# Kernel tuning notes

Hardware: AMD Instinct MI355X
Metric: run time of the kernel (lower is better)

Reference implementation:

```python
import jax, jax.numpy as jnp
import numpy as np

B, S, D, H = 4, 2048, 1024, 16
HD = D // H  # head_dim = 64


def setup_inputs() -> dict:
    key = jax.random.key(0)
    ks = jax.random.split(key, 5)
    scale = 0.02
    x = jax.random.normal(ks[0], (B, S, D), dtype=jnp.float32)
    W_qkv = jax.random.normal(ks[1], (D, 3 * D), dtype=jnp.float32) * scale
    b_qkv = jnp.zeros((3 * D,), dtype=jnp.float32)
    W_out = jax.random.normal(ks[2], (D, D), dtype=jnp.float32) * scale
    b_out = jnp.zeros((D,), dtype=jnp.float32)
    return {"x": x, "W_qkv": W_qkv, "b_qkv": b_qkv, "W_out": W_out, "b_out": b_out}


def reference(x, W_qkv, b_qkv, W_out, b_out):
    b, s, d = x.shape
    qkv = x @ W_qkv + b_qkv                      # [B,S,3D]
    q, k, v = jnp.split(qkv, 3, axis=-1)
    # [B,S,D] -> [B,H,S,hd]
    q = q.reshape(b, s, H, HD).transpose(0, 2, 1, 3)
    k = k.reshape(b, s, H, HD).transpose(0, 2, 1, 3)
    v = v.reshape(b, s, H, HD).transpose(0, 2, 1, 3)
    scores = jnp.einsum('bhqd,bhkd->bhqk', q, k) / jnp.sqrt(jnp.float32(HD))
    causal = jnp.tril(jnp.ones((s, s), dtype=bool))  # [S,S]
    scores = jnp.where(causal[None, None], scores, -jnp.inf)
    probs = jax.nn.softmax(scores, axis=-1)
    # dropout is identity in eval mode
    attn = jnp.einsum('bhqk,bhkd->bhqd', probs, v)  # [B,H,S,hd]
    attn = attn.transpose(0, 2, 1, 3).reshape(b, s, d)
    return attn @ W_out + b_out
```

## Files before the change

kernel.cpp:

```cpp
#include <hip/hip_runtime.h>


typedef short s16;
typedef __attribute__((ext_vector_type(4))) short s16x4;
typedef __attribute__((ext_vector_type(8))) short bf16x8;
typedef __attribute__((ext_vector_type(4))) float f32x4;

__device__ __forceinline__ s16 f2bf(float f) {
    union { float f; unsigned int i; } v;
    v.f = f;
    unsigned int r = v.i + 0x7fffu + ((v.i >> 16) & 1u);
    return (s16)(r >> 16);
}

__device__ __forceinline__ unsigned pack_bf16(float a, float b) {
    union { float f; unsigned u; } x, y;
    x.f = a; y.f = b;
    return __byte_perm(x.u + 0x8000u, y.u + 0x8000u, 0x7632);
}

__device__ __forceinline__ void load_lds16(const s16* g, s16* lds_base) {
    __builtin_amdgcn_global_load_lds(
        (const __attribute__((address_space(1))) void*)g,
        (__attribute__((address_space(3))) void*)lds_base, 16, 0, 0);
}

__global__ void cast_f32_bf16(const float* __restrict__ in, s16* __restrict__ out) {
    const int i = (blockIdx.x * 256 + threadIdx.x) * 4;
    const float4 f = *(const float4*)(in + i);
    s16x4 r = {f2bf(f.x), f2bf(f.y), f2bf(f.z), f2bf(f.w)};
    *(s16x4*)(out + i) = r;
}

__global__ void transpose_cast(const float* __restrict__ in,
                               s16* __restrict__ out, int R, int C) {
    __shared__ float tile[32][33];
    const int cb = blockIdx.x * 32, rb = blockIdx.y * 32;
    const int tx = threadIdx.x, ty = threadIdx.y;
#pragma unroll
    for (int i = 0; i < 32; i += 8)
        tile[ty + i][tx] = in[(size_t)(rb + ty + i) * C + cb + tx];
    __syncthreads();
#pragma unroll
    for (int i = 0; i < 32; i += 8)
        out[(size_t)(cb + ty + i) * R + rb + tx] = f2bf(tile[tx][ty + i]);
}

template <bool OUT_F32>
__global__ __launch_bounds__(512, 2) void gemm_bt_bias_256(
    const s16* __restrict__ A,
    const s16* __restrict__ Bt,
    const float* __restrict__ bias,
    void* __restrict__ Cv,
    int M, int N, int K, int gx) {
    __shared__ __attribute__((aligned(16))) s16 As[2][256 * 64];
    __shared__ __attribute__((aligned(16))) s16 Bs[2][256 * 64];

    const int tid  = threadIdx.x;
    const int lane = tid & 63;
    const int wave = tid >> 6;
    const int l15  = lane & 15;
    const int quad = lane >> 4;
    const int wr   = wave >> 2;
    const int wc   = wave & 3;

    const int cpx = (int)gridDim.x >> 3;
    const int bid = (int)blockIdx.x;
    const int swz = (bid & 7) * cpx + (bid >> 3);
    const int m0 = (swz / gx) * 256;
    const int n0 = (swz % gx) * 256;

    const int srow = tid >> 3;
    const int sg   = (tid & 7) ^ (srow & 7);
    const s16* Ag = A  + (size_t)(m0 + srow) * K + sg * 8;
    const s16* Bg = Bt + (size_t)(n0 + srow) * K + sg * 8;

#define STG(buf, c, kt) do {                                                        \
    load_lds16(Ag + (size_t)(c) * 64 * K + (size_t)(kt) * 64,                       \
               &As[buf][(c) * 4096 + wave * 512]);                                  \
    load_lds16(Bg + (size_t)(c) * 64 * K + (size_t)(kt) * 64,                       \
               &Bs[buf][(c) * 4096 + wave * 512]); } while (0)

    f32x4 acc[8][4];
#pragma unroll
    for (int i = 0; i < 8; ++i)
#pragma unroll
        for (int j = 0; j < 4; ++j)
            acc[i][j] = (f32x4){0.f, 0.f, 0.f, 0.f};

    const int nk = K >> 6;

    STG(0, 0, 0); STG(0, 1, 0); STG(0, 2, 0); STG(0, 3, 0);
    __syncthreads();

    for (int t = 0; t < nk; ++t) {
        const int buf  = t & 1;
        const int nbuf = buf ^ 1;
        const bool pre = (t + 1 < nk);
        bf16x8 bfr[4][2];
#pragma unroll
        for (int q = 0; q < 4; ++q) {
            if (q == 0) {
#pragma unroll
                for (int n = 0; n < 4; ++n)
#pragma unroll
                    for (int ks = 0; ks < 2; ++ks) {
                        const int br = wc * 64 + n * 16 + l15;
                        const int gs = ((ks * 4 + quad) ^ (l15 & 7)) * 8;
                        bfr[n][ks] = *(const bf16x8*)(&Bs[buf][br * 64 + gs]);
                    }
            }
            bf16x8 af[2][2];
#pragma unroll
            for (int i = 0; i < 2; ++i)
#pragma unroll
                for (int ks = 0; ks < 2; ++ks) {
                    const int ar = wr * 128 + (q * 2 + i) * 16 + l15;
                    const int gs = ((ks * 4 + quad) ^ (l15 & 7)) * 8;
                    af[i][ks] = *(const bf16x8*)(&As[buf][ar * 64 + gs]);
                }
            if (q == 0 && pre) { STG(nbuf, 0, t + 1); STG(nbuf, 1, t + 1); }
            if (q == 1 && pre) { STG(nbuf, 2, t + 1); STG(nbuf, 3, t + 1); }
            __builtin_amdgcn_s_barrier();
            __builtin_amdgcn_s_setprio(1);
#pragma unroll
            for (int i = 0; i < 2; ++i)
#pragma unroll
                for (int n = 0; n < 4; ++n)
#pragma unroll
                    for (int ks = 0; ks < 2; ++ks)
                        acc[q * 2 + i][n] = __builtin_amdgcn_mfma_f32_16x16x32_bf16(
                            af[i][ks], bfr[n][ks], acc[q * 2 + i][n], 0, 0, 0);
            __builtin_amdgcn_s_setprio(0);
            if (q == 3)
                __syncthreads();
            else
                __builtin_amdgcn_s_barrier();
        }
    }
#undef STG

#pragma unroll
    for (int n = 0; n < 4; ++n) {
        const int col = n0 + wc * 64 + n * 16 + l15;
        const float bv = bias[col];
#pragma unroll
        for (int mf = 0; mf < 8; ++mf) {
            const int rowb = m0 + wr * 128 + mf * 16 + quad * 4;
#pragma unroll
            for (int r = 0; r < 4; ++r) {
                const float v = acc[mf][n][r] + bv;
                if constexpr (OUT_F32)
                    ((float*)Cv)[(size_t)(rowb + r) * N + col] = v;
                else
                    ((s16*)Cv)[(size_t)(rowb + r) * N + col] = f2bf(v);
            }
        }
    }
}

__global__ __launch_bounds__(256) void attn_fwd(
    const s16* __restrict__ qkv,
    s16* __restrict__ attn) {
    __shared__ __attribute__((aligned(16))) s16 Ks[64 * 72];
    __shared__ __attribute__((aligned(16))) s16 Vt[64 * 72];
    __shared__ __attribute__((aligned(16))) s16 PT[4][32][88];

    const int tid  = threadIdx.x;
    const int lane = tid & 63;
    const int wave = tid >> 6;
    const int l15  = lane & 15;
    const int quad = lane >> 4;

    const int bid = blockIdx.x;
    const int hi  = bid >> 8;
    const int a   = bid & 3;
    const int bh  = (bid >> 2) & 63;
    const int qbase = a * 2 + (hi >> 1);
    const int qt  = (hi & 1) ? 15 - qbase : qbase;

    const size_t rowbase = (size_t)(bh >> 4) * 2048;
    const int hoff = (bh & 15) * 64;
    const int kp  = tid >> 3;
    const int p_s = tid & 7;
    const int kg  = kp >> 2;

    const float C2 = 0.18033688011112042f;
    const float M2 = 12.0f;

    const int wq = qt * 128 + wave * 32;

    bf16x8 qf[2][2];
#pragma unroll
    for (int qs = 0; qs < 2; ++qs)
#pragma unroll
        for (int ks = 0; ks < 2; ++ks)
            qf[qs][ks] = *(const bf16x8*)(qkv + (rowbase + wq + qs * 16 + l15) * 3072 + hoff + ks * 32 + quad * 8);

    float l_lane[2] = {0.f, 0.f};
    f32x4 o[2][4];
#pragma unroll
    for (int qs = 0; qs < 2; ++qs)
#pragma unroll
        for (int hs = 0; hs < 4; ++hs)
            o[qs][hs] = (f32x4){0.f, 0.f, 0.f, 0.f};

    const int nkt = qt * 2 + 2;
    bf16x8 kv[2], vv[2];
#pragma unroll
    for (int dk = 0; dk < 2; ++dk) {
        const s16* g = qkv + (rowbase + 2 * kp + dk) * 3072 + hoff + p_s * 8;
        kv[dk] = *(const bf16x8*)(g + 1024);
        vv[dk] = *(const bf16x8*)(g + 2048);
    }

    for (int kt = 0; kt < nkt; ++kt) {
        const int k0 = kt * 64;
        __syncthreads();
#pragma unroll
        for (int dk = 0; dk < 2; ++dk)
            *(bf16x8*)(Ks + (2 * kp + dk) * 72 + p_s * 8) = kv[dk];
#pragma unroll
        for (int j = 0; j < 8; ++j) {
            const unsigned dw = (unsigned)(unsigned short)vv[0][j] |
                                ((unsigned)(unsigned short)vv[1][j] << 16);
            *(unsigned*)(Vt + (p_s * 8 + j) * 72 + ((kg ^ p_s) << 3) + (2 * kp & 7)) = dw;
        }
        __syncthreads();

        if (kt + 1 < nkt) {
#pragma unroll
            for (int dk = 0; dk < 2; ++dk) {
                const s16* g = qkv + (rowbase + k0 + 64 + 2 * kp + dk) * 3072 + hoff + p_s * 8;
                kv[dk] = *(const bf16x8*)(g + 1024);
                vv[dk] = *(const bf16x8*)(g + 2048);
            }
        }

        if (k0 > wq + 31) continue;

        f32x4 st[2][4];
#pragma unroll
        for (int qs = 0; qs < 2; ++qs)
#pragma unroll
            for (int kb = 0; kb < 4; ++kb)
                st[qs][kb] = (f32x4){0.f, 0.f, 0.f, 0.f};
        __builtin_amdgcn_s_setprio(1);
#pragma unroll
        for (int kb = 0; kb < 4; ++kb)
#pragma unroll
            for (int ks = 0; ks < 2; ++ks) {
                const bf16x8 kf = *(const bf16x8*)(Ks + (kb * 16 + l15) * 72 + ks * 32 + quad * 8);
#pragma unroll
                for (int qs = 0; qs < 2; ++qs)
                    st[qs][kb] = __builtin_amdgcn_mfma_f32_16x16x32_bf16(kf, qf[qs][ks], st[qs][kb], 0, 0, 0);
            }
        __builtin_amdgcn_s_setprio(0);

        const bool edge = (k0 + 63 > wq);
#pragma unroll
        for (int qs = 0; qs < 2; ++qs) {
            const int q = wq + qs * 16 + l15;
#pragma unroll
            for (int kb = 0; kb < 4; ++kb) {
                float p4[4];
#pragma unroll
                for (int r = 0; r < 4; ++r) {
                    float t = fmaf(st[qs][kb][r], C2, -M2);
                    if (edge) {
                        const int key = k0 + kb * 16 + quad * 4 + r;
                        t = (key <= q) ? t : -150.f;
                    }
                    p4[r] = __builtin_amdgcn_exp2f(t);
                    l_lane[qs] += p4[r];
                }
                uint2 dd;
                dd.x = pack_bf16(p4[0], p4[1]);
                dd.y = pack_bf16(p4[2], p4[3]);
                *(uint2*)(&PT[wave][qs * 16 + l15][kb * 16 + quad * 4]) = dd;
            }
        }

        __builtin_amdgcn_s_setprio(1);
#pragma unroll
        for (int kk = 0; kk < 2; ++kk) {
            bf16x8 pf[2];
#pragma unroll
            for (int qs = 0; qs < 2; ++qs)
                pf[qs] = *(const bf16x8*)(&PT[wave][qs * 16 + l15][kk * 32 + quad * 8]);
#pragma unroll
            for (int hs = 0; hs < 4; ++hs) {
                const bf16x8 vf = *(const bf16x8*)(
                    Vt + (hs * 16 + l15) * 72 + (((kk * 4 + quad) ^ (2 * hs + (l15 >> 3))) << 3));
#pragma unroll
                for (int qs = 0; qs < 2; ++qs)
                    o[qs][hs] = __builtin_amdgcn_mfma_f32_16x16x32_bf16(vf, pf[qs], o[qs][hs], 0, 0, 0);
            }
        }
        __builtin_amdgcn_s_setprio(0);
    }

    float rl[2];
#pragma unroll
    for (int qs = 0; qs < 2; ++qs) {
        float l = l_lane[qs];
        l += __shfl_xor(l, 16);
        l += __shfl_xor(l, 32);
        rl[qs] = 1.f / l;
    }

#pragma unroll
    for (int qs = 0; qs < 2; ++qs) {
        const int q = wq + qs * 16 + l15;
#pragma unroll
        for (int hs = 0; hs < 4; ++hs) {
            uint2 dd;
            dd.x = pack_bf16(o[qs][hs][0] * rl[qs], o[qs][hs][1] * rl[qs]);
            dd.y = pack_bf16(o[qs][hs][2] * rl[qs], o[qs][hs][3] * rl[qs]);
            *(uint2*)(attn + (rowbase + q) * 1024 + hoff + hs * 16 + quad * 4) = dd;
        }
    }
}

extern "C" void kernel_launch(void* const* d_in, const int* in_sizes, int n_in,
                              void* d_out, int out_size, void* d_ws, size_t ws_size,
                              hipStream_t stream) {
    const float* x    = (const float*)d_in[0];
    const float* Wqkv = (const float*)d_in[1];
    const float* bqkv = (const float*)d_in[2];
    const float* Wout = (const float*)d_in[3];
    const float* bout = (const float*)d_in[4];
    float* out = (float*)d_out;

    s16* ws   = (s16*)d_ws;
    s16* qkv  = ws;
    s16* xba  = qkv + (size_t)8192 * 3072;
    s16* wtq  = xba + (size_t)8192 * 1024;
    s16* wto  = wtq + (size_t)3072 * 1024;

    cast_f32_bf16<<<8192, 256, 0, stream>>>(x, xba);
    transpose_cast<<<dim3(3072 / 32, 1024 / 32), dim3(32, 8), 0, stream>>>(Wqkv, wtq, 1024, 3072);
    transpose_cast<<<dim3(1024 / 32, 1024 / 32), dim3(32, 8), 0, stream>>>(Wout, wto, 1024, 1024);
    gemm_bt_bias_256<false><<<384, 512, 0, stream>>>(
        xba, wtq, bqkv, qkv, 8192, 3072, 1024, 12);
    attn_fwd<<<1024, 256, 0, stream>>>(qkv, xba);
    gemm_bt_bias_256<true><<<128, 512, 0, stream>>>(
        xba, wto, bout, out, 8192, 1024, 1024, 4);
}
```

Baseline: 268.8 us.

## Replace GEMM full syncs with staged vmcnt waits and reorder tile loads

The GEMM main loop now issues the B-tile loads first, then the A-tile chunks in the order 0,2,1,3, so each wave-row's first half arrives early. Full __syncthreads (which drain all outstanding loads) are replaced by partial s_waitcnt vmcnt counts plus plain barriers. The next iteration can then start on the first A chunks while the last two are still in flight. The epilogue store loop is also reordered so the four column fragments of a row are written back-to-back, with the bias values hoisted. The risk is that the hand-counted vmcnt values must exactly match the number of loads issued per thread, or stale LDS data will be read.

```diff
diff --git a/kernel.cpp b/kernel.cpp
--- a/kernel.cpp
+++ b/kernel.cpp
@@ -75,11 +75,10 @@
     const s16* Ag = A  + (size_t)(m0 + srow) * K + sg * 8;
     const s16* Bg = Bt + (size_t)(n0 + srow) * K + sg * 8;
 
-#define STG(buf, c, kt) do {                                                        \
-    load_lds16(Ag + (size_t)(c) * 64 * K + (size_t)(kt) * 64,                       \
-               &As[buf][(c) * 4096 + wave * 512]);                                  \
-    load_lds16(Bg + (size_t)(c) * 64 * K + (size_t)(kt) * 64,                       \
-               &Bs[buf][(c) * 4096 + wave * 512]); } while (0)
+#define STG_A(buf, c, kt) load_lds16(Ag + (size_t)(c) * 64 * K + (size_t)(kt) * 64, \
+                                     &As[buf][(c) * 4096 + wave * 512])
+#define STG_B(buf, c, kt) load_lds16(Bg + (size_t)(c) * 64 * K + (size_t)(kt) * 64, \
+                                     &Bs[buf][(c) * 4096 + wave * 512])
 
     f32x4 acc[8][4];
 #pragma unroll
@@ -90,8 +89,10 @@
 
     const int nk = K >> 6;
 
-    STG(0, 0, 0); STG(0, 1, 0); STG(0, 2, 0); STG(0, 3, 0);
-    __syncthreads();
+    STG_B(0, 0, 0); STG_B(0, 1, 0); STG_B(0, 2, 0); STG_B(0, 3, 0);
+    STG_A(0, 0, 0); STG_A(0, 2, 0); STG_A(0, 1, 0); STG_A(0, 3, 0);
+    asm volatile("s_waitcnt vmcnt(2)" ::: "memory");
+    __builtin_amdgcn_s_barrier();
 
     for (int t = 0; t < nk; ++t) {
         const int buf  = t & 1;
@@ -119,8 +120,14 @@
                     const int gs = ((ks * 4 + quad) ^ (l15 & 7)) * 8;
                     af[i][ks] = *(const bf16x8*)(&As[buf][ar * 64 + gs]);
                 }
-            if (q == 0 && pre) { STG(nbuf, 0, t + 1); STG(nbuf, 1, t + 1); }
-            if (q == 1 && pre) { STG(nbuf, 2, t + 1); STG(nbuf, 3, t + 1); }
+            if (q == 0 && pre) {
+                STG_B(nbuf, 0, t + 1); STG_B(nbuf, 1, t + 1);
+                STG_B(nbuf, 2, t + 1); STG_B(nbuf, 3, t + 1);
+            }
+            if (q == 1 && pre) {
+                STG_A(nbuf, 0, t + 1); STG_A(nbuf, 2, t + 1);
+                STG_A(nbuf, 1, t + 1); STG_A(nbuf, 3, t + 1);
+            }
             __builtin_amdgcn_s_barrier();
             __builtin_amdgcn_s_setprio(1);
 #pragma unroll
@@ -132,28 +139,35 @@
                         acc[q * 2 + i][n] = __builtin_amdgcn_mfma_f32_16x16x32_bf16(
                             af[i][ks], bfr[n][ks], acc[q * 2 + i][n], 0, 0, 0);
             __builtin_amdgcn_s_setprio(0);
-            if (q == 3)
-                __syncthreads();
-            else
-                __builtin_amdgcn_s_barrier();
-        }
-    }
-#undef STG
-
-#pragma unroll
-    for (int n = 0; n < 4; ++n) {
-        const int col = n0 + wc * 64 + n * 16 + l15;
-        const float bv = bias[col];
-#pragma unroll
-        for (int mf = 0; mf < 8; ++mf) {
-            const int rowb = m0 + wr * 128 + mf * 16 + quad * 4;
-#pragma unroll
-            for (int r = 0; r < 4; ++r) {
-                const float v = acc[mf][n][r] + bv;
+            if (q == 1) {
+                if (pre) asm volatile("s_waitcnt vmcnt(8)" ::: "memory");
+                else     asm volatile("s_waitcnt vmcnt(0)" ::: "memory");
+            }
+            if (q == 3 && pre)
+                asm volatile("s_waitcnt vmcnt(2)" ::: "memory");
+            __builtin_amdgcn_s_barrier();
+        }
+    }
+#undef STG_A
+#undef STG_B
+
+    float bv[4];
+#pragma unroll
+    for (int n = 0; n < 4; ++n)
+        bv[n] = bias[n0 + wc * 64 + n * 16 + l15];
+#pragma unroll
+    for (int mf = 0; mf < 8; ++mf) {
+#pragma unroll
+        for (int r = 0; r < 4; ++r) {
+            const int row = m0 + wr * 128 + mf * 16 + quad * 4 + r;
+#pragma unroll
+            for (int n = 0; n < 4; ++n) {
+                const int col = n0 + wc * 64 + n * 16 + l15;
+                const float v = acc[mf][n][r] + bv[n];
                 if constexpr (OUT_F32)
-                    ((float*)Cv)[(size_t)(rowb + r) * N + col] = v;
+                    ((float*)Cv)[(size_t)row * N + col] = v;
                 else
-                    ((s16*)Cv)[(size_t)(rowb + r) * N + col] = f2bf(v);
+                    ((s16*)Cv)[(size_t)row * N + col] = f2bf(v);
             }
         }
     }
```

Result: slower. 274.5 us (+2.1%).
